# Kernel optimization log

Hardware: AMD Instinct MI355X
Metric: run time of the kernel (lower is better)

## Reference

```python
import jax, jax.numpy as jnp
import numpy as np

N_NODES = 100000
N_EDGES = 3200000
IN_DIM = 62
OUT_DIM = 16
EDGE_DIM = 2


def setup_inputs() -> dict:
    key = jax.random.key(0)
    ks = jax.random.split(key, 8)
    h = jax.random.normal(ks[0], (N_NODES, IN_DIM), dtype=jnp.float32)
    e = jax.random.normal(ks[1], (N_EDGES, EDGE_DIM), dtype=jnp.float32)
    src = jax.random.randint(ks[2], (N_EDGES,), 0, N_NODES, dtype=jnp.int32)
    dst = jax.random.randint(ks[3], (N_EDGES,), 0, N_NODES, dtype=jnp.int32)
    # xavier-normal-ish scaled weights
    W_fc = jax.random.normal(ks[4], (OUT_DIM, IN_DIM), dtype=jnp.float32) * 0.2
    W_attn = jax.random.normal(ks[5], (1, 2 * OUT_DIM + EDGE_DIM), dtype=jnp.float32) * 0.2
    W_edge = jax.random.normal(ks[6], (EDGE_DIM, EDGE_DIM), dtype=jnp.float32) * 0.5
    W_e2n = jax.random.normal(ks[7], (OUT_DIM, EDGE_DIM), dtype=jnp.float32) * 0.5
    return {"h": h, "e": e, "src": src, "dst": dst, "W_fc": W_fc,
            "W_attn": W_attn, "W_edge": W_edge, "W_e2n": W_e2n}


def _agat_forward(h, e, src, dst, W_fc, W_attn, W_edge, W_e2n):
    n = h.shape[0]
    d = W_fc.shape[0]
    z = h @ W_fc.T                      # [N, D]
    ex = e @ W_edge.T                   # [E, edge_dim]
    # attn_fc([z_src, z_dst, ex]) split into per-part projections
    Wa_src = W_attn[:, :d]              # [1, D]
    Wa_dst = W_attn[:, d:2 * d]         # [1, D]
    Wa_e = W_attn[:, 2 * d:]            # [1, edge_dim]
    a_src = (z @ Wa_src.T)[:, 0]        # [N] per-node, gathered per-edge
    a_dst = (z @ Wa_dst.T)[:, 0]        # [N]
    a = a_src[src] + a_dst[dst] + (ex @ Wa_e.T)[:, 0]   # [E]
    e_att = jax.nn.leaky_relu(a, negative_slope=0.01)    # [E]
    # segment softmax over incoming edges of each dst node
    m = jax.ops.segment_max(e_att, dst, num_segments=n)  # [N]
    w = jnp.exp(e_att - m[dst])                           # [E]
    denom = jax.ops.segment_sum(w, dst, num_segments=n)   # [N]
    attn = w / denom[dst]                                  # [E]
    # message = z_src + ez; aggregated as attn-weighted sum (matches
    # sum(attn*z) + sum(attn*ez) in reduce_func)
    ez = ex @ W_e2n.T                                      # [E, D]
    msg = attn[:, None] * (z[src] + ez)                    # [E, D]
    return jax.ops.segment_sum(msg, dst, num_segments=n)   # [N, D]


def reference(h, e, src, dst, W_fc, W_attn, W_edge, W_e2n):
    return _agat_forward(h, e, src, dst, W_fc, W_attn, W_edge, W_e2n)
```

## Files before the change

### kernel.cpp

```cpp
#include <hip/hip_runtime.h>
#include <hip/hip_fp16.h>

#define N_NODES 100000
#define N_EDGES 3200000
#define IN_DIM  62
#define OUT_DIM 16

#define EBC    6144
#define EPT    (EBC / 1024)
#define NEB    ((N_EDGES + EBC - 1) / EBC)
#define NPB    ((N_NODES + 1023) / 1024)
#define NBUCK  ((N_NODES + 63) / 64)
#define CSTR   16
#define ACCS   21
#define SZF    1048576.0f
#define SWF    16777216.0f
#define GTH    256

typedef int nat_i2 __attribute__((ext_vector_type(2)));

__device__ __forceinline__ unsigned fkey(float f) {
    unsigned b = __float_as_uint(f);
    return (b & 0x80000000u) ? ~b : (b | 0x80000000u);
}
__device__ __forceinline__ float finv(unsigned u) {
    unsigned b = (u & 0x80000000u) ? (u ^ 0x80000000u) : ~u;
    return __uint_as_float(b);
}

__global__ __launch_bounds__(1024) void proj_append_kernel(
    const float* __restrict__ h,
    const float* __restrict__ W_fc,
    const float* __restrict__ W_attn,
    const float* __restrict__ e,
    const int*   __restrict__ src,
    const int*   __restrict__ dst,
    __half* __restrict__ zh,
    float* __restrict__ a_src_arr,
    float* __restrict__ a_dst_arr,
    int*   __restrict__ cursor,
    nat_i2* __restrict__ records,
    int cap)
{
    __shared__ int  cnt[NBUCK];
    __shared__ int  pfx[NBUCK];
    __shared__ int  combo[NBUCK];
    __shared__ int2 pay[EBC];
    __shared__ unsigned short pbkt[EBC];
    __shared__ int  wsum[16];

    int tid = threadIdx.x;

    if (blockIdx.x < NPB) {
        int i = blockIdx.x * 1024 + tid;
        if (i >= N_NODES) return;

        float acc[OUT_DIM];
#pragma unroll
        for (int j = 0; j < OUT_DIM; ++j) acc[j] = 0.f;

        const float2* __restrict__ hr = (const float2*)(h + (size_t)i * IN_DIM);
#pragma unroll
        for (int kk = 0; kk < IN_DIM / 2; ++kk) {
            float2 hv = hr[kk];
#pragma unroll
            for (int j = 0; j < OUT_DIM; ++j) {
                acc[j] += hv.x * W_fc[j * IN_DIM + 2 * kk]
                        + hv.y * W_fc[j * IN_DIM + 2 * kk + 1];
            }
        }

        float asrc = 0.f, adst = 0.f;
#pragma unroll
        for (int j = 0; j < OUT_DIM; ++j) {
            asrc += acc[j] * W_attn[j];
            adst += acc[j] * W_attn[OUT_DIM + j];
        }

        union { __half hx[16]; uint4 q[2]; } u;
#pragma unroll
        for (int j = 0; j < OUT_DIM; ++j) u.hx[j] = __float2half(acc[j]);
        uint4* __restrict__ zrow = (uint4*)(zh + (size_t)i * OUT_DIM);
        zrow[0] = u.q[0];
        zrow[1] = u.q[1];

        a_src_arr[i] = asrc;
        a_dst_arr[i] = adst;
        return;
    }

    int be = blockIdx.x - NPB;
    long ebase = (long)be * EBC;
    int chunk_n = (int)min((long)EBC, (long)N_EDGES - ebase);

    int dv[EPT], sv[EPT];
    float2 ev[EPT];
#pragma unroll
    for (int j = 0; j < EPT; ++j) {
        int p = tid + j * 1024;
        dv[j] = -1;
        if (p < chunk_n) {
            long eid = ebase + p;
            dv[j] = dst[eid];
            sv[j] = src[eid];
            ev[j] = ((const float2*)e)[eid];
        }
    }

    for (int t = tid; t < NBUCK; t += 1024) cnt[t] = 0;
    __syncthreads();

#pragma unroll
    for (int j = 0; j < EPT; ++j)
        if (dv[j] >= 0) atomicAdd(&cnt[dv[j] >> 6], 1);
    __syncthreads();

    int b0 = 2 * tid, b1 = b0 + 1;
    int c0 = (b0 < NBUCK) ? cnt[b0] : 0;
    int c1 = (b1 < NBUCK) ? cnt[b1] : 0;
    if (b0 < NBUCK) cnt[b0] = 0;
    if (b1 < NBUCK) cnt[b1] = 0;
    int gb0 = 0, gb1 = 0;
    if (c0) gb0 = atomicAdd(&cursor[b0 * CSTR], c0);
    if (c1) gb1 = atomicAdd(&cursor[b1 * CSTR], c1);

    int ts = c0 + c1;
    {
        int lane = tid & 63, wid = tid >> 6;
        int x = ts;
#pragma unroll
        for (int off = 1; off < 64; off <<= 1) {
            int y = __shfl_up(x, off, 64);
            if (lane >= off) x += y;
        }
        if (lane == 63) wsum[wid] = x;
        __syncthreads();
        if (wid == 0) {
            int v = (lane < 16) ? wsum[lane] : 0;
#pragma unroll
            for (int off = 1; off < 16; off <<= 1) {
                int y = __shfl_up(v, off, 64);
                if (lane >= off) v += y;
            }
            if (lane < 16) wsum[lane] = v;
        }
        __syncthreads();
        int texcl = x - ts + (wid ? wsum[wid - 1] : 0);
        if (b0 < NBUCK) { pfx[b0] = texcl;      combo[b0] = b0 * cap + gb0 - texcl; }
        if (b1 < NBUCK) { pfx[b1] = texcl + c0; combo[b1] = b1 * cap + gb1 - (texcl + c0); }
    }
    __syncthreads();

#pragma unroll
    for (int j = 0; j < EPT; ++j) {
        if (dv[j] >= 0) {
            int b = dv[j] >> 6;
            union { __half2 h2; int i; } uu;
            uu.h2.x = __float2half(ev[j].x);
            uu.h2.y = __float2half(ev[j].y);
            int r = atomicAdd(&cnt[b], 1);
            int q = pfx[b] + r;
            pay[q]  = make_int2(uu.i, sv[j] | ((dv[j] & 63) << 17));
            pbkt[q] = (unsigned short)b;
        }
    }
    __syncthreads();

    for (int p = tid; p < chunk_n; p += 1024) {
        int2 v = pay[p];
        int bb = pbkt[p];
        int pos = combo[bb] + p;
        if (pos < (bb + 1) * cap) {
            nat_i2 vv; vv.x = v.x; vv.y = v.y;
            __builtin_nontemporal_store(vv, records + pos);
        }
    }
}

__global__ __launch_bounds__(GTH) void gather_fx_kernel(
    const int*    __restrict__ cursor,
    const nat_i2* __restrict__ records,
    const __half* __restrict__ zh,
    const float*  __restrict__ a_src_arr,
    const float*  __restrict__ a_dst_arr,
    const float*  __restrict__ W_attn,
    const float*  __restrict__ W_edge,
    const float*  __restrict__ W_e2n,
    float* __restrict__ out, int cap)
{
    __shared__ unsigned maxv[64];
    __shared__ int      acci[64 * ACCS];
    __shared__ float    adst_l[64];
    __shared__ float    we2n_s[2 * OUT_DIM];

    int b   = blockIdx.x;
    int tid = threadIdx.x;
    long lo = (long)b * cap;
    int n   = cursor[b * CSTR];
    int nl  = n < cap ? n : cap;

    if (tid < 64) {
        maxv[tid] = 0u;
        int node = (b << 6) + tid;
        adst_l[tid] = (node < N_NODES) ? a_dst_arr[node] : 0.f;
    }
    if (tid < 2 * OUT_DIM) we2n_s[tid] = W_e2n[tid];
    for (int t = tid; t < 64 * ACCS; t += GTH) acci[t] = 0;
    __syncthreads();

    float we00 = W_edge[0], we01 = W_edge[1], we10 = W_edge[2], we11 = W_edge[3];
    float wa0  = W_attn[2 * OUT_DIM], wa1 = W_attn[2 * OUT_DIM + 1];

    for (int k = tid; k < nl; k += GTH) {
        nat_i2 r = records[lo + k];
        int s  = r.y & 0x1FFFF;
        int ld = (r.y >> 17) & 63;
        union { int i; __half2 h2; } ue; ue.i = r.x;
        float e0 = __low2float(ue.h2), e1 = __high2float(ue.h2);
        float ex0 = e0 * we00 + e1 * we01;
        float ex1 = e0 * we10 + e1 * we11;
        float a  = a_src_arr[s] + adst_l[ld] + ex0 * wa0 + ex1 * wa1;
        float ea = (a > 0.f) ? a : 0.01f * a;
        atomicMax(&maxv[ld], fkey(ea));
    }
    __syncthreads();

    for (int k = tid; k < nl; k += GTH) {
        nat_i2 r = records[lo + k];
        int s  = r.y & 0x1FFFF;
        int ld = (r.y >> 17) & 63;
        union { int i; __half2 h2; } ue; ue.i = r.x;
        float e0 = __low2float(ue.h2), e1 = __high2float(ue.h2);
        float ex0 = e0 * we00 + e1 * we01;
        float ex1 = e0 * we10 + e1 * we11;
        float a  = a_src_arr[s] + adst_l[ld] + ex0 * wa0 + ex1 * wa1;
        float ea = (a > 0.f) ? a : 0.01f * a;
        float m  = finv(maxv[ld]);
        float w  = __expf(ea - m);

        const uint4* __restrict__ zr = (const uint4*)(zh + (size_t)s * OUT_DIM);
        uint4 z0 = zr[0], z1 = zr[1];

        int* ab = acci + ld * ACCS;
        union { unsigned u; __half2 h2; } t2;
        float ws = w * SZF;
        t2.u = z0.x; atomicAdd(ab + 0,  __float2int_rn(ws * __low2float(t2.h2)));
                     atomicAdd(ab + 1,  __float2int_rn(ws * __high2float(t2.h2)));
        t2.u = z0.y; atomicAdd(ab + 2,  __float2int_rn(ws * __low2float(t2.h2)));
                     atomicAdd(ab + 3,  __float2int_rn(ws * __high2float(t2.h2)));
        t2.u = z0.z; atomicAdd(ab + 4,  __float2int_rn(ws * __low2float(t2.h2)));
                     atomicAdd(ab + 5,  __float2int_rn(ws * __high2float(t2.h2)));
        t2.u = z0.w; atomicAdd(ab + 6,  __float2int_rn(ws * __low2float(t2.h2)));
                     atomicAdd(ab + 7,  __float2int_rn(ws * __high2float(t2.h2)));
        t2.u = z1.x; atomicAdd(ab + 8,  __float2int_rn(ws * __low2float(t2.h2)));
                     atomicAdd(ab + 9,  __float2int_rn(ws * __high2float(t2.h2)));
        t2.u = z1.y; atomicAdd(ab + 10, __float2int_rn(ws * __low2float(t2.h2)));
                     atomicAdd(ab + 11, __float2int_rn(ws * __high2float(t2.h2)));
        t2.u = z1.z; atomicAdd(ab + 12, __float2int_rn(ws * __low2float(t2.h2)));
                     atomicAdd(ab + 13, __float2int_rn(ws * __high2float(t2.h2)));
        t2.u = z1.w; atomicAdd(ab + 14, __float2int_rn(ws * __low2float(t2.h2)));
                     atomicAdd(ab + 15, __float2int_rn(ws * __high2float(t2.h2)));
        atomicAdd(ab + 16, __float2int_rn(w * SWF));
        atomicAdd(ab + 17, __float2int_rn(ws * ex0));
        atomicAdd(ab + 18, __float2int_rn(ws * ex1));
    }
    __syncthreads();

#pragma unroll
    for (int rp = 0; rp < 4; ++rp) {
        int idx  = rp * GTH + tid;
        int ln   = idx >> 4;
        int j    = idx & 15;
        int node = (b << 6) + ln;
        if (node < N_NODES) {
            const int* ab = acci + ln * ACCS;
            int swi = ab[16];
            float num  = (float)ab[j]  * (1.f / SZF);
            float ex0s = (float)ab[17] * (1.f / SZF);
            float ex1s = (float)ab[18] * (1.f / SZF);
            float ez   = ex0s * we2n_s[2 * j] + ex1s * we2n_s[2 * j + 1];
            float iv   = (swi != 0) ? (SWF / (float)swi) : 0.f;
            out[(size_t)node * OUT_DIM + j] = (num + ez) * iv;
        }
    }
}


__global__ __launch_bounds__(256) void node_proj_fb_kernel(
    const float* __restrict__ h,
    const float* __restrict__ W_fc,
    const float* __restrict__ W_attn,
    float* __restrict__ z,
    float* __restrict__ a_src_arr,
    float* __restrict__ a_dst_arr,
    float* __restrict__ denom,
    float* __restrict__ out)
{
    int i = blockIdx.x * blockDim.x + threadIdx.x;
    if (i >= N_NODES) return;

    float acc[OUT_DIM];
#pragma unroll
    for (int j = 0; j < OUT_DIM; ++j) acc[j] = 0.f;

    const float2* __restrict__ hr = (const float2*)(h + (size_t)i * IN_DIM);
#pragma unroll
    for (int kk = 0; kk < IN_DIM / 2; ++kk) {
        float2 hv = hr[kk];
#pragma unroll
        for (int j = 0; j < OUT_DIM; ++j) {
            acc[j] += hv.x * W_fc[j * IN_DIM + 2 * kk]
                    + hv.y * W_fc[j * IN_DIM + 2 * kk + 1];
        }
    }

    float asrc = 0.f, adst = 0.f;
#pragma unroll
    for (int j = 0; j < OUT_DIM; ++j) {
        asrc += acc[j] * W_attn[j];
        adst += acc[j] * W_attn[OUT_DIM + j];
    }

    float4* __restrict__ zrow = (float4*)(z + (size_t)i * OUT_DIM);
    zrow[0] = make_float4(acc[0],  acc[1],  acc[2],  acc[3]);
    zrow[1] = make_float4(acc[4],  acc[5],  acc[6],  acc[7]);
    zrow[2] = make_float4(acc[8],  acc[9],  acc[10], acc[11]);
    zrow[3] = make_float4(acc[12], acc[13], acc[14], acc[15]);

    a_src_arr[i] = asrc;
    a_dst_arr[i] = adst;
    denom[i] = 0.f;

    float4 z4 = make_float4(0.f, 0.f, 0.f, 0.f);
    float4* __restrict__ orow = (float4*)(out + (size_t)i * OUT_DIM);
    orow[0] = z4; orow[1] = z4; orow[2] = z4; orow[3] = z4;
}

__global__ __launch_bounds__(256) void edge_kernel(
    const float* __restrict__ e,
    const int*   __restrict__ src,
    const int*   __restrict__ dst,
    const float* __restrict__ W_attn,
    const float* __restrict__ W_edge,
    const float* __restrict__ W_e2n,
    const float* __restrict__ z,
    const float* __restrict__ a_src_arr,
    const float* __restrict__ a_dst_arr,
    float* __restrict__ denom,
    float* __restrict__ out)
{
    int eid = blockIdx.x * blockDim.x + threadIdx.x;
    if (eid >= N_EDGES) return;

    int s = src[eid];
    int d = dst[eid];

    float2 ev = ((const float2*)e)[eid];
    float ex0 = ev.x * W_edge[0] + ev.y * W_edge[1];
    float ex1 = ev.x * W_edge[2] + ev.y * W_edge[3];

    float a = a_src_arr[s] + a_dst_arr[d]
            + ex0 * W_attn[2 * OUT_DIM] + ex1 * W_attn[2 * OUT_DIM + 1];
    float ea = (a > 0.f) ? a : 0.01f * a;
    float w  = __expf(ea);

    unsafeAtomicAdd(denom + d, w);

    const float4* __restrict__ zrow = (const float4*)(z + (size_t)s * OUT_DIM);
    float4 z0 = zrow[0], z1 = zrow[1], z2 = zrow[2], z3 = zrow[3];

    float* __restrict__ orow = out + (size_t)d * OUT_DIM;
    float zs[OUT_DIM] = { z0.x, z0.y, z0.z, z0.w,
                          z1.x, z1.y, z1.z, z1.w,
                          z2.x, z2.y, z2.z, z2.w,
                          z3.x, z3.y, z3.z, z3.w };
#pragma unroll
    for (int j = 0; j < OUT_DIM; ++j) {
        float ez = ex0 * W_e2n[2 * j] + ex1 * W_e2n[2 * j + 1];
        unsafeAtomicAdd(orow + j, w * (zs[j] + ez));
    }
}

__global__ __launch_bounds__(256) void normalize_kernel(
    float* __restrict__ out, const float* __restrict__ denom)
{
    int tid = blockIdx.x * blockDim.x + threadIdx.x;
    const int total = N_NODES * OUT_DIM / 4;
    if (tid >= total) return;
    int n = tid >> 2;
    float dn = denom[n];
    float inv = (dn != 0.f) ? (1.f / dn) : 0.f;
    float4 v = ((float4*)out)[tid];
    v.x *= inv; v.y *= inv; v.z *= inv; v.w *= inv;
    ((float4*)out)[tid] = v;
}

extern "C" void kernel_launch(void* const* d_in, const int* in_sizes, int n_in,
                              void* d_out, int out_size, void* d_ws, size_t ws_size,
                              hipStream_t stream)
{
    const float* h      = (const float*)d_in[0];
    const float* e      = (const float*)d_in[1];
    const int*   src    = (const int*)  d_in[2];
    const int*   dst    = (const int*)  d_in[3];
    const float* W_fc   = (const float*)d_in[4];
    const float* W_attn = (const float*)d_in[5];
    const float* W_edge = (const float*)d_in[6];
    const float* W_e2n  = (const float*)d_in[7];
    float* out = (float*)d_out;

    char* ws = (char*)d_ws;

    size_t off = 0;
    __half* zh        = (__half*)(ws + off); off += (size_t)N_NODES * OUT_DIM * 2;
    float*  a_src_arr = (float*) (ws + off); off += (size_t)N_NODES * 4;
    float*  a_dst_arr = (float*) (ws + off); off += (size_t)N_NODES * 4;
    off = (off + 255) & ~(size_t)255;
    int*    cursor = (int*)(ws + off);
    size_t  cur_bytes = (size_t)NBUCK * CSTR * 4;
    off += (cur_bytes + 255) & ~(size_t)255;
    size_t rec_off = (off + 255) & ~(size_t)255;

    int cap = 0;
    if      (ws_size >= rec_off + (size_t)NBUCK * 4096 * 8) cap = 4096;
    else if (ws_size >= rec_off + (size_t)NBUCK * 3072 * 8) cap = 3072;
    else if (ws_size >= rec_off + (size_t)NBUCK * 2560 * 8) cap = 2560;
    else if (ws_size >= rec_off + (size_t)NBUCK * 2304 * 8) cap = 2304;

    if (cap) {
        nat_i2* records = (nat_i2*)(ws + rec_off);

        hipMemsetAsync(cursor, 0, cur_bytes, stream);

        proj_append_kernel<<<NPB + NEB, 1024, 0, stream>>>(
            h, W_fc, W_attn, e, src, dst,
            zh, a_src_arr, a_dst_arr, cursor, records, cap);

        gather_fx_kernel<<<NBUCK, GTH, 0, stream>>>(
            cursor, records, zh, a_src_arr, a_dst_arr,
            W_attn, W_edge, W_e2n, out, cap);
    } else {
        size_t foff = 0;
        float* z     = (float*)(ws + foff); foff += (size_t)N_NODES * OUT_DIM * 4;
        float* asrc  = (float*)(ws + foff); foff += (size_t)N_NODES * 4;
        float* adst  = (float*)(ws + foff); foff += (size_t)N_NODES * 4;
        float* denom = (float*)(ws + foff); foff += (size_t)N_NODES * 4;

        node_proj_fb_kernel<<<(N_NODES + 255) / 256, 256, 0, stream>>>(
            h, W_fc, W_attn, z, asrc, adst, denom, out);

        edge_kernel<<<(N_EDGES + 255) / 256, 256, 0, stream>>>(
            e, src, dst, W_attn, W_edge, W_e2n, z, asrc, adst, denom, out);

        normalize_kernel<<<(N_NODES * OUT_DIM / 4 + 255) / 256, 256, 0, stream>>>(
            out, denom);
    }
}
```

Measured before the change: 225.5 us.

## Fuse projection, bucketing and gather into one cooperative persistent kernel

Replaces the memset plus two-kernel pipeline with a single cooperative kernel. It zeroes the cursors, runs projection and edge bucketing in a grid-stride loop, syncs the grid, then runs the per-bucket gather. Buckets grow from 64 to 256 destination nodes with a larger per-bucket capacity, and blocks shrink to 256 threads with 2048-edge chunks. This removes launch gaps and the memset, but adds grid-sync cost and fewer, heavier gather blocks (391) with a large shared accumulator that may limit occupancy.

```diff
diff --git a/kernel.cpp b/kernel.cpp
--- a/kernel.cpp
+++ b/kernel.cpp
@@ -1,21 +1,26 @@
 #include <hip/hip_runtime.h>
 #include <hip/hip_fp16.h>
+#include <hip/hip_cooperative_groups.h>
+
+namespace cg = cooperative_groups;
 
 #define N_NODES 100000
 #define N_EDGES 3200000
 #define IN_DIM  62
 #define OUT_DIM 16
 
-#define EBC    6144
-#define EPT    (EBC / 1024)
+#define BTH    256
+#define EBC    2048
+#define EPT    8
 #define NEB    ((N_EDGES + EBC - 1) / EBC)
-#define NPB    ((N_NODES + 1023) / 1024)
-#define NBUCK  ((N_NODES + 63) / 64)
+#define BNODES 256
+#define NB2    ((N_NODES + BNODES - 1) / BNODES)
+#define NPU    NB2
 #define CSTR   16
 #define ACCS   21
 #define SZF    1048576.0f
 #define SWF    16777216.0f
-#define GTH    256
+#define NCU    256
 
 typedef int nat_i2 __attribute__((ext_vector_type(2)));
 
@@ -28,68 +33,73 @@
     return __uint_as_float(b);
 }
 
-__global__ __launch_bounds__(1024) void proj_append_kernel(
-    const float* __restrict__ h,
-    const float* __restrict__ W_fc,
+struct AppendSh {
+    int  cnt[NB2];
+    int  pfx[NB2];
+    int  combo[NB2];
+    int2 pay[EBC];
+    unsigned short pbkt[EBC];
+    int  wsum[BTH / 64];
+};
+struct GatherSh {
+    unsigned maxv[BNODES];
+    int      acci[BNODES * ACCS];
+    float    adst_l[BNODES];
+    float    we2n[2 * OUT_DIM];
+};
+union ShArena { AppendSh a; GatherSh g; };
+
+__device__ __forceinline__ void do_proj(
+    int u, int tid,
+    const float* __restrict__ h, const float* __restrict__ W_fc,
     const float* __restrict__ W_attn,
-    const float* __restrict__ e,
-    const int*   __restrict__ src,
-    const int*   __restrict__ dst,
-    __half* __restrict__ zh,
-    float* __restrict__ a_src_arr,
-    float* __restrict__ a_dst_arr,
-    int*   __restrict__ cursor,
-    nat_i2* __restrict__ records,
-    int cap)
-{
-    __shared__ int  cnt[NBUCK];
-    __shared__ int  pfx[NBUCK];
-    __shared__ int  combo[NBUCK];
-    __shared__ int2 pay[EBC];
-    __shared__ unsigned short pbkt[EBC];
-    __shared__ int  wsum[16];
-
-    int tid = threadIdx.x;
-
-    if (blockIdx.x < NPB) {
-        int i = blockIdx.x * 1024 + tid;
-        if (i >= N_NODES) return;
-
-        float acc[OUT_DIM];
-#pragma unroll
-        for (int j = 0; j < OUT_DIM; ++j) acc[j] = 0.f;
-
-        const float2* __restrict__ hr = (const float2*)(h + (size_t)i * IN_DIM);
-#pragma unroll
-        for (int kk = 0; kk < IN_DIM / 2; ++kk) {
-            float2 hv = hr[kk];
-#pragma unroll
-            for (int j = 0; j < OUT_DIM; ++j) {
-                acc[j] += hv.x * W_fc[j * IN_DIM + 2 * kk]
-                        + hv.y * W_fc[j * IN_DIM + 2 * kk + 1];
-            }
-        }
-
-        float asrc = 0.f, adst = 0.f;
+    __half* __restrict__ zh, float* __restrict__ a_src_arr,
+    float* __restrict__ a_dst_arr)
+{
+    int i = u * BTH + tid;
+    if (i >= N_NODES) return;
+
+    float acc[OUT_DIM];
+#pragma unroll
+    for (int j = 0; j < OUT_DIM; ++j) acc[j] = 0.f;
+
+    const float2* __restrict__ hr = (const float2*)(h + (size_t)i * IN_DIM);
+#pragma unroll
+    for (int kk = 0; kk < IN_DIM / 2; ++kk) {
+        float2 hv = hr[kk];
 #pragma unroll
         for (int j = 0; j < OUT_DIM; ++j) {
-            asrc += acc[j] * W_attn[j];
-            adst += acc[j] * W_attn[OUT_DIM + j];
-        }
-
-        union { __half hx[16]; uint4 q[2]; } u;
-#pragma unroll
-        for (int j = 0; j < OUT_DIM; ++j) u.hx[j] = __float2half(acc[j]);
-        uint4* __restrict__ zrow = (uint4*)(zh + (size_t)i * OUT_DIM);
-        zrow[0] = u.q[0];
-        zrow[1] = u.q[1];
-
-        a_src_arr[i] = asrc;
-        a_dst_arr[i] = adst;
-        return;
-    }
-
-    int be = blockIdx.x - NPB;
+            acc[j] += hv.x * W_fc[j * IN_DIM + 2 * kk]
+                    + hv.y * W_fc[j * IN_DIM + 2 * kk + 1];
+        }
+    }
+
+    float asrc = 0.f, adst = 0.f;
+#pragma unroll
+    for (int j = 0; j < OUT_DIM; ++j) {
+        asrc += acc[j] * W_attn[j];
+        adst += acc[j] * W_attn[OUT_DIM + j];
+    }
+
+    union { __half hx[16]; uint4 q[2]; } uq;
+#pragma unroll
+    for (int j = 0; j < OUT_DIM; ++j) uq.hx[j] = __float2half(acc[j]);
+    uint4* __restrict__ zrow = (uint4*)(zh + (size_t)i * OUT_DIM);
+    zrow[0] = uq.q[0];
+    zrow[1] = uq.q[1];
+
+    a_src_arr[i] = asrc;
+    a_dst_arr[i] = adst;
+}
+
+__device__ __forceinline__ void do_append(
+    int be, int tid, AppendSh& S,
+    const float* __restrict__ e, const int* __restrict__ src,
+    const int* __restrict__ dst, int* __restrict__ cursor,
+    nat_i2* __restrict__ records, int cap)
+{
+    __syncthreads();
+
     long ebase = (long)be * EBC;
     int chunk_n = (int)min((long)EBC, (long)N_EDGES - ebase);
 
@@ -97,7 +107,7 @@
     float2 ev[EPT];
 #pragma unroll
     for (int j = 0; j < EPT; ++j) {
-        int p = tid + j * 1024;
+        int p = tid + j * BTH;
         dv[j] = -1;
         if (p < chunk_n) {
             long eid = ebase + p;
@@ -107,19 +117,19 @@
         }
     }
 
-    for (int t = tid; t < NBUCK; t += 1024) cnt[t] = 0;
+    for (int t = tid; t < NB2; t += BTH) S.cnt[t] = 0;
     __syncthreads();
 
 #pragma unroll
     for (int j = 0; j < EPT; ++j)
-        if (dv[j] >= 0) atomicAdd(&cnt[dv[j] >> 6], 1);
+        if (dv[j] >= 0) atomicAdd(&S.cnt[dv[j] >> 8], 1);
     __syncthreads();
 
     int b0 = 2 * tid, b1 = b0 + 1;
-    int c0 = (b0 < NBUCK) ? cnt[b0] : 0;
-    int c1 = (b1 < NBUCK) ? cnt[b1] : 0;
-    if (b0 < NBUCK) cnt[b0] = 0;
-    if (b1 < NBUCK) cnt[b1] = 0;
+    int c0 = (b0 < NB2) ? S.cnt[b0] : 0;
+    int c1 = (b1 < NB2) ? S.cnt[b1] : 0;
+    if (b0 < NB2) S.cnt[b0] = 0;
+    if (b1 < NB2) S.cnt[b1] = 0;
     int gb0 = 0, gb1 = 0;
     if (c0) gb0 = atomicAdd(&cursor[b0 * CSTR], c0);
     if (c1) gb1 = atomicAdd(&cursor[b1 * CSTR], c1);
@@ -133,43 +143,41 @@
             int y = __shfl_up(x, off, 64);
             if (lane >= off) x += y;
         }
-        if (lane == 63) wsum[wid] = x;
+        if (lane == 63) S.wsum[wid] = x;
         __syncthreads();
-        if (wid == 0) {
-            int v = (lane < 16) ? wsum[lane] : 0;
-#pragma unroll
-            for (int off = 1; off < 16; off <<= 1) {
-                int y = __shfl_up(v, off, 64);
-                if (lane >= off) v += y;
+        if (tid == 0) {
+            int run = 0;
+#pragma unroll
+            for (int i2 = 0; i2 < BTH / 64; ++i2) {
+                int t = S.wsum[i2]; S.wsum[i2] = run; run += t;
             }
-            if (lane < 16) wsum[lane] = v;
         }
         __syncthreads();
-        int texcl = x - ts + (wid ? wsum[wid - 1] : 0);
-        if (b0 < NBUCK) { pfx[b0] = texcl;      combo[b0] = b0 * cap + gb0 - texcl; }
-        if (b1 < NBUCK) { pfx[b1] = texcl + c0; combo[b1] = b1 * cap + gb1 - (texcl + c0); }
+        int texcl = x - ts + S.wsum[wid];
+        if (b0 < NB2) { S.pfx[b0] = texcl;      S.combo[b0] = b0 * cap + gb0 - texcl; }
+        if (b1 < NB2) { S.pfx[b1] = texcl + c0; S.combo[b1] = b1 * cap + gb1 - (texcl + c0); }
     }
     __syncthreads();
 
 #pragma unroll
     for (int j = 0; j < EPT; ++j) {
         if (dv[j] >= 0) {
-            int b = dv[j] >> 6;
+            int b = dv[j] >> 8;
             union { __half2 h2; int i; } uu;
             uu.h2.x = __float2half(ev[j].x);
             uu.h2.y = __float2half(ev[j].y);
-            int r = atomicAdd(&cnt[b], 1);
-            int q = pfx[b] + r;
-            pay[q]  = make_int2(uu.i, sv[j] | ((dv[j] & 63) << 17));
-            pbkt[q] = (unsigned short)b;
-        }
-    }
-    __syncthreads();
-
-    for (int p = tid; p < chunk_n; p += 1024) {
-        int2 v = pay[p];
-        int bb = pbkt[p];
-        int pos = combo[bb] + p;
+            int r = atomicAdd(&S.cnt[b], 1);
+            int q = S.pfx[b] + r;
+            S.pay[q]  = make_int2(uu.i, sv[j] | ((dv[j] & (BNODES - 1)) << 17));
+            S.pbkt[q] = (unsigned short)b;
+        }
+    }
+    __syncthreads();
+
+    for (int p = tid; p < chunk_n; p += BTH) {
+        int2 v  = S.pay[p];
+        int  bb = S.pbkt[p];
+        int pos = S.combo[bb] + p;
         if (pos < (bb + 1) * cap) {
             nat_i2 vv; vv.x = v.x; vv.y = v.y;
             __builtin_nontemporal_store(vv, records + pos);
@@ -177,71 +185,63 @@
     }
 }
 
-__global__ __launch_bounds__(GTH) void gather_fx_kernel(
-    const int*    __restrict__ cursor,
-    const nat_i2* __restrict__ records,
-    const __half* __restrict__ zh,
-    const float*  __restrict__ a_src_arr,
-    const float*  __restrict__ a_dst_arr,
-    const float*  __restrict__ W_attn,
-    const float*  __restrict__ W_edge,
-    const float*  __restrict__ W_e2n,
+__device__ __forceinline__ void do_gather(
+    int b, int tid, GatherSh& G,
+    const int* __restrict__ cursor, const nat_i2* __restrict__ records,
+    const __half* __restrict__ zh, const float* __restrict__ a_src_arr,
+    const float* __restrict__ a_dst_arr, const float* __restrict__ W_attn,
+    const float* __restrict__ W_edge, const float* __restrict__ W_e2n,
     float* __restrict__ out, int cap)
 {
-    __shared__ unsigned maxv[64];
-    __shared__ int      acci[64 * ACCS];
-    __shared__ float    adst_l[64];
-    __shared__ float    we2n_s[2 * OUT_DIM];
-
-    int b   = blockIdx.x;
-    int tid = threadIdx.x;
+    __syncthreads();
+
     long lo = (long)b * cap;
     int n   = cursor[b * CSTR];
     int nl  = n < cap ? n : cap;
 
-    if (tid < 64) {
-        maxv[tid] = 0u;
-        int node = (b << 6) + tid;
-        adst_l[tid] = (node < N_NODES) ? a_dst_arr[node] : 0.f;
-    }
-    if (tid < 2 * OUT_DIM) we2n_s[tid] = W_e2n[tid];
-    for (int t = tid; t < 64 * ACCS; t += GTH) acci[t] = 0;
+    {
+        G.maxv[tid] = 0u;
+        int node = b * BNODES + tid;
+        G.adst_l[tid] = (node < N_NODES) ? a_dst_arr[node] : 0.f;
+        if (tid < 2 * OUT_DIM) G.we2n[tid] = W_e2n[tid];
+        for (int t = tid; t < BNODES * ACCS; t += BTH) G.acci[t] = 0;
+    }
     __syncthreads();
 
     float we00 = W_edge[0], we01 = W_edge[1], we10 = W_edge[2], we11 = W_edge[3];
     float wa0  = W_attn[2 * OUT_DIM], wa1 = W_attn[2 * OUT_DIM + 1];
 
-    for (int k = tid; k < nl; k += GTH) {
+    for (int k = tid; k < nl; k += BTH) {
         nat_i2 r = records[lo + k];
         int s  = r.y & 0x1FFFF;
-        int ld = (r.y >> 17) & 63;
+        int ld = (r.y >> 17) & 255;
         union { int i; __half2 h2; } ue; ue.i = r.x;
         float e0 = __low2float(ue.h2), e1 = __high2float(ue.h2);
         float ex0 = e0 * we00 + e1 * we01;
         float ex1 = e0 * we10 + e1 * we11;
-        float a  = a_src_arr[s] + adst_l[ld] + ex0 * wa0 + ex1 * wa1;
+        float a  = a_src_arr[s] + G.adst_l[ld] + ex0 * wa0 + ex1 * wa1;
         float ea = (a > 0.f) ? a : 0.01f * a;
-        atomicMax(&maxv[ld], fkey(ea));
-    }
-    __syncthreads();
-
-    for (int k = tid; k < nl; k += GTH) {
+        atomicMax(&G.maxv[ld], fkey(ea));
+    }
+    __syncthreads();
+
+    for (int k = tid; k < nl; k += BTH) {
         nat_i2 r = records[lo + k];
         int s  = r.y & 0x1FFFF;
-        int ld = (r.y >> 17) & 63;
+        int ld = (r.y >> 17) & 255;
         union { int i; __half2 h2; } ue; ue.i = r.x;
         float e0 = __low2float(ue.h2), e1 = __high2float(ue.h2);
         float ex0 = e0 * we00 + e1 * we01;
         float ex1 = e0 * we10 + e1 * we11;
-        float a  = a_src_arr[s] + adst_l[ld] + ex0 * wa0 + ex1 * wa1;
+        float a  = a_src_arr[s] + G.adst_l[ld] + ex0 * wa0 + ex1 * wa1;
         float ea = (a > 0.f) ? a : 0.01f * a;
-        float m  = finv(maxv[ld]);
+        float m  = finv(G.maxv[ld]);
         float w  = __expf(ea - m);
 
         const uint4* __restrict__ zr = (const uint4*)(zh + (size_t)s * OUT_DIM);
         uint4 z0 = zr[0], z1 = zr[1];
 
-        int* ab = acci + ld * ACCS;
+        int* ab = G.acci + ld * ACCS;
         union { unsigned u; __half2 h2; } t2;
         float ws = w * SZF;
         t2.u = z0.x; atomicAdd(ab + 0,  __float2int_rn(ws * __low2float(t2.h2)));
@@ -267,22 +267,77 @@
     __syncthreads();
 
 #pragma unroll
-    for (int rp = 0; rp < 4; ++rp) {
-        int idx  = rp * GTH + tid;
+    for (int rp = 0; rp < 16; ++rp) {
+        int idx  = rp * BTH + tid;
         int ln   = idx >> 4;
         int j    = idx & 15;
-        int node = (b << 6) + ln;
+        int node = b * BNODES + ln;
         if (node < N_NODES) {
-            const int* ab = acci + ln * ACCS;
+            const int* ab = G.acci + ln * ACCS;
             int swi = ab[16];
             float num  = (float)ab[j]  * (1.f / SZF);
             float ex0s = (float)ab[17] * (1.f / SZF);
             float ex1s = (float)ab[18] * (1.f / SZF);
-            float ez   = ex0s * we2n_s[2 * j] + ex1s * we2n_s[2 * j + 1];
+            float ez   = ex0s * G.we2n[2 * j] + ex1s * G.we2n[2 * j + 1];
             float iv   = (swi != 0) ? (SWF / (float)swi) : 0.f;
             out[(size_t)node * OUT_DIM + j] = (num + ez) * iv;
         }
     }
+}
+
+__global__ __launch_bounds__(BTH) void fused_kernel(
+    const float* __restrict__ h, const float* __restrict__ e,
+    const int* __restrict__ src, const int* __restrict__ dst,
+    const float* __restrict__ W_fc, const float* __restrict__ W_attn,
+    const float* __restrict__ W_edge, const float* __restrict__ W_e2n,
+    __half* __restrict__ zh, float* __restrict__ a_src_arr,
+    float* __restrict__ a_dst_arr, int* __restrict__ cursor,
+    nat_i2* __restrict__ records, float* __restrict__ out, int cap)
+{
+    __shared__ ShArena sh;
+    cg::grid_group grid = cg::this_grid();
+    int tid = threadIdx.x;
+
+    for (int t = blockIdx.x * BTH + tid; t < NB2 * CSTR; t += gridDim.x * BTH)
+        cursor[t] = 0;
+    grid.sync();
+
+    for (int u = blockIdx.x; u < NPU + NEB; u += gridDim.x) {
+        if (u < NPU) do_proj(u, tid, h, W_fc, W_attn, zh, a_src_arr, a_dst_arr);
+        else         do_append(u - NPU, tid, sh.a, e, src, dst, cursor, records, cap);
+    }
+    grid.sync();
+
+    for (int b = blockIdx.x; b < NB2; b += gridDim.x)
+        do_gather(b, tid, sh.g, cursor, records, zh, a_src_arr, a_dst_arr,
+                  W_attn, W_edge, W_e2n, out, cap);
+}
+
+__global__ __launch_bounds__(BTH) void proj_append_kernel(
+    const float* __restrict__ h, const float* __restrict__ W_fc,
+    const float* __restrict__ W_attn, const float* __restrict__ e,
+    const int* __restrict__ src, const int* __restrict__ dst,
+    __half* __restrict__ zh, float* __restrict__ a_src_arr,
+    float* __restrict__ a_dst_arr, int* __restrict__ cursor,
+    nat_i2* __restrict__ records, int cap)
+{
+    __shared__ AppendSh sh;
+    if (blockIdx.x < NPU)
+        do_proj(blockIdx.x, threadIdx.x, h, W_fc, W_attn, zh, a_src_arr, a_dst_arr);
+    else
+        do_append(blockIdx.x - NPU, threadIdx.x, sh, e, src, dst, cursor, records, cap);
+}
+
+__global__ __launch_bounds__(BTH) void gather_kernel(
+    const int* __restrict__ cursor, const nat_i2* __restrict__ records,
+    const __half* __restrict__ zh, const float* __restrict__ a_src_arr,
+    const float* __restrict__ a_dst_arr, const float* __restrict__ W_attn,
+    const float* __restrict__ W_edge, const float* __restrict__ W_e2n,
+    float* __restrict__ out, int cap)
+{
+    __shared__ GatherSh sh;
+    do_gather(blockIdx.x, threadIdx.x, sh, cursor, records, zh,
+              a_src_arr, a_dst_arr, W_attn, W_edge, W_e2n, out, cap);
 }
 
 
@@ -417,28 +472,47 @@
     float*  a_dst_arr = (float*) (ws + off); off += (size_t)N_NODES * 4;
     off = (off + 255) & ~(size_t)255;
     int*    cursor = (int*)(ws + off);
-    size_t  cur_bytes = (size_t)NBUCK * CSTR * 4;
+    size_t  cur_bytes = (size_t)NB2 * CSTR * 4;
     off += (cur_bytes + 255) & ~(size_t)255;
     size_t rec_off = (off + 255) & ~(size_t)255;
 
     int cap = 0;
-    if      (ws_size >= rec_off + (size_t)NBUCK * 4096 * 8) cap = 4096;
-    else if (ws_size >= rec_off + (size_t)NBUCK * 3072 * 8) cap = 3072;
-    else if (ws_size >= rec_off + (size_t)NBUCK * 2560 * 8) cap = 2560;
-    else if (ws_size >= rec_off + (size_t)NBUCK * 2304 * 8) cap = 2304;
+    if      (ws_size >= rec_off + (size_t)NB2 * 12288 * 8) cap = 12288;
+    else if (ws_size >= rec_off + (size_t)NB2 * 10240 * 8) cap = 10240;
+    else if (ws_size >= rec_off + (size_t)NB2 * 9216 * 8)  cap = 9216;
+    else if (ws_size >= rec_off + (size_t)NB2 * 8704 * 8)  cap = 8704;
 
     if (cap) {
         nat_i2* records = (nat_i2*)(ws + rec_off);
 
-        hipMemsetAsync(cursor, 0, cur_bytes, stream);
-
-        proj_append_kernel<<<NPB + NEB, 1024, 0, stream>>>(
-            h, W_fc, W_attn, e, src, dst,
-            zh, a_src_arr, a_dst_arr, cursor, records, cap);
-
-        gather_fx_kernel<<<NBUCK, GTH, 0, stream>>>(
-            cursor, records, zh, a_src_arr, a_dst_arr,
-            W_attn, W_edge, W_e2n, out, cap);
+        hipError_t lerr = hipErrorUnknown;
+        int maxB = 0;
+        hipError_t qerr = hipOccupancyMaxActiveBlocksPerMultiprocessor(
+            &maxB, reinterpret_cast<const void*>(fused_kernel), BTH, 0);
+        if (qerr == hipSuccess && maxB > 0) {
+            int gridB = maxB * NCU;
+            if (gridB > NPU + NEB) gridB = NPU + NEB;
+            void* kargs[] = {
+                (void*)&h, (void*)&e, (void*)&src, (void*)&dst,
+                (void*)&W_fc, (void*)&W_attn, (void*)&W_edge, (void*)&W_e2n,
+                (void*)&zh, (void*)&a_src_arr, (void*)&a_dst_arr,
+                (void*)&cursor, (void*)&records, (void*)&out, (void*)&cap };
+            lerr = hipLaunchCooperativeKernel(
+                reinterpret_cast<const void*>(fused_kernel),
+                dim3(gridB), dim3(BTH), kargs, 0, stream);
+        }
+
+        if (lerr != hipSuccess) {
+            hipMemsetAsync(cursor, 0, cur_bytes, stream);
+
+            proj_append_kernel<<<NPU + NEB, BTH, 0, stream>>>(
+                h, W_fc, W_attn, e, src, dst,
+                zh, a_src_arr, a_dst_arr, cursor, records, cap);
+
+            gather_kernel<<<NB2, BTH, 0, stream>>>(
+                cursor, records, zh, a_src_arr, a_dst_arr,
+                W_attn, W_edge, W_e2n, out, cap);
+        }
     } else {
         size_t foff = 0;
         float* z     = (float*)(ws + foff); foff += (size_t)N_NODES * OUT_DIM * 4;
```

After: 347.3 us. +54.0%, slower.

## Cache bucket edge records and attention scores in registers across softmax passes

Applied to the files above, without the earlier changes.

The per-bucket gather kernel now loads up to 16 edge records per thread into registers once, with a nontemporal load, and keeps the computed leaky-relu scores. The second pass reuses them instead of re-reading records and a_src from global memory and recomputing the score. It also batches the a_src gathers to expose memory-level parallelism. It assumes each bucket holds at most 16*256 records, and the added register arrays could lower occupancy.

```diff
diff --git a/kernel.cpp b/kernel.cpp
--- a/kernel.cpp
+++ b/kernel.cpp
@@ -16,6 +16,7 @@
 #define SZF    1048576.0f
 #define SWF    16777216.0f
 #define GTH    256
+#define EPTG   16
 
 typedef int nat_i2 __attribute__((ext_vector_type(2)));
 
@@ -211,58 +212,82 @@
     float we00 = W_edge[0], we01 = W_edge[1], we10 = W_edge[2], we11 = W_edge[3];
     float wa0  = W_attn[2 * OUT_DIM], wa1 = W_attn[2 * OUT_DIM + 1];
 
-    for (int k = tid; k < nl; k += GTH) {
-        nat_i2 r = records[lo + k];
-        int s  = r.y & 0x1FFFF;
-        int ld = (r.y >> 17) & 63;
-        union { int i; __half2 h2; } ue; ue.i = r.x;
-        float e0 = __low2float(ue.h2), e1 = __high2float(ue.h2);
-        float ex0 = e0 * we00 + e1 * we01;
-        float ex1 = e0 * we10 + e1 * we11;
-        float a  = a_src_arr[s] + adst_l[ld] + ex0 * wa0 + ex1 * wa1;
-        float ea = (a > 0.f) ? a : 0.01f * a;
-        atomicMax(&maxv[ld], fkey(ea));
-    }
-    __syncthreads();
-
-    for (int k = tid; k < nl; k += GTH) {
-        nat_i2 r = records[lo + k];
-        int s  = r.y & 0x1FFFF;
-        int ld = (r.y >> 17) & 63;
-        union { int i; __half2 h2; } ue; ue.i = r.x;
-        float e0 = __low2float(ue.h2), e1 = __high2float(ue.h2);
-        float ex0 = e0 * we00 + e1 * we01;
-        float ex1 = e0 * we10 + e1 * we11;
-        float a  = a_src_arr[s] + adst_l[ld] + ex0 * wa0 + ex1 * wa1;
-        float ea = (a > 0.f) ? a : 0.01f * a;
-        float m  = finv(maxv[ld]);
-        float w  = __expf(ea - m);
-
-        const uint4* __restrict__ zr = (const uint4*)(zh + (size_t)s * OUT_DIM);
-        uint4 z0 = zr[0], z1 = zr[1];
-
-        int* ab = acci + ld * ACCS;
-        union { unsigned u; __half2 h2; } t2;
-        float ws = w * SZF;
-        t2.u = z0.x; atomicAdd(ab + 0,  __float2int_rn(ws * __low2float(t2.h2)));
-                     atomicAdd(ab + 1,  __float2int_rn(ws * __high2float(t2.h2)));
-        t2.u = z0.y; atomicAdd(ab + 2,  __float2int_rn(ws * __low2float(t2.h2)));
-                     atomicAdd(ab + 3,  __float2int_rn(ws * __high2float(t2.h2)));
-        t2.u = z0.z; atomicAdd(ab + 4,  __float2int_rn(ws * __low2float(t2.h2)));
-                     atomicAdd(ab + 5,  __float2int_rn(ws * __high2float(t2.h2)));
-        t2.u = z0.w; atomicAdd(ab + 6,  __float2int_rn(ws * __low2float(t2.h2)));
-                     atomicAdd(ab + 7,  __float2int_rn(ws * __high2float(t2.h2)));
-        t2.u = z1.x; atomicAdd(ab + 8,  __float2int_rn(ws * __low2float(t2.h2)));
-                     atomicAdd(ab + 9,  __float2int_rn(ws * __high2float(t2.h2)));
-        t2.u = z1.y; atomicAdd(ab + 10, __float2int_rn(ws * __low2float(t2.h2)));
-                     atomicAdd(ab + 11, __float2int_rn(ws * __high2float(t2.h2)));
-        t2.u = z1.z; atomicAdd(ab + 12, __float2int_rn(ws * __low2float(t2.h2)));
-                     atomicAdd(ab + 13, __float2int_rn(ws * __high2float(t2.h2)));
-        t2.u = z1.w; atomicAdd(ab + 14, __float2int_rn(ws * __low2float(t2.h2)));
-                     atomicAdd(ab + 15, __float2int_rn(ws * __high2float(t2.h2)));
-        atomicAdd(ab + 16, __float2int_rn(w * SWF));
-        atomicAdd(ab + 17, __float2int_rn(ws * ex0));
-        atomicAdd(ab + 18, __float2int_rn(ws * ex1));
+    int   ry[EPTG];
+    int   eh[EPTG];
+    float ea[EPTG];
+
+#pragma unroll
+    for (int j = 0; j < EPTG; ++j) ry[j] = -1;
+
+#pragma unroll
+    for (int j = 0; j < EPTG; ++j) {
+        int k = tid + j * GTH;
+        if (k < nl) {
+            nat_i2 r = __builtin_nontemporal_load(records + lo + k);
+            ry[j] = r.y;
+            eh[j] = r.x;
+        }
+    }
+
+    float av[EPTG];
+#pragma unroll
+    for (int j = 0; j < EPTG; ++j)
+        if (ry[j] >= 0) av[j] = a_src_arr[ry[j] & 0x1FFFF];
+
+#pragma unroll
+    for (int j = 0; j < EPTG; ++j) {
+        if (ry[j] >= 0) {
+            int ld = (ry[j] >> 17) & 63;
+            union { int i; __half2 h2; } ue; ue.i = eh[j];
+            float e0 = __low2float(ue.h2), e1 = __high2float(ue.h2);
+            float ex0 = e0 * we00 + e1 * we01;
+            float ex1 = e0 * we10 + e1 * we11;
+            float a  = av[j] + adst_l[ld] + ex0 * wa0 + ex1 * wa1;
+            float eaj = (a > 0.f) ? a : 0.01f * a;
+            ea[j] = eaj;
+            atomicMax(&maxv[ld], fkey(eaj));
+        }
+    }
+    __syncthreads();
+
+#pragma unroll
+    for (int j = 0; j < EPTG; ++j) {
+        if (ry[j] >= 0) {
+            int s  = ry[j] & 0x1FFFF;
+            int ld = (ry[j] >> 17) & 63;
+            union { int i; __half2 h2; } ue; ue.i = eh[j];
+            float e0 = __low2float(ue.h2), e1 = __high2float(ue.h2);
+            float ex0 = e0 * we00 + e1 * we01;
+            float ex1 = e0 * we10 + e1 * we11;
+            float m = finv(maxv[ld]);
+            float w = __expf(ea[j] - m);
+
+            const uint4* __restrict__ zr = (const uint4*)(zh + (size_t)s * OUT_DIM);
+            uint4 z0 = zr[0], z1 = zr[1];
+
+            int* ab = acci + ld * ACCS;
+            union { unsigned u; __half2 h2; } t2;
+            float ws = w * SZF;
+            t2.u = z0.x; atomicAdd(ab + 0,  __float2int_rn(ws * __low2float(t2.h2)));
+                         atomicAdd(ab + 1,  __float2int_rn(ws * __high2float(t2.h2)));
+            t2.u = z0.y; atomicAdd(ab + 2,  __float2int_rn(ws * __low2float(t2.h2)));
+                         atomicAdd(ab + 3,  __float2int_rn(ws * __high2float(t2.h2)));
+            t2.u = z0.z; atomicAdd(ab + 4,  __float2int_rn(ws * __low2float(t2.h2)));
+                         atomicAdd(ab + 5,  __float2int_rn(ws * __high2float(t2.h2)));
+            t2.u = z0.w; atomicAdd(ab + 6,  __float2int_rn(ws * __low2float(t2.h2)));
+                         atomicAdd(ab + 7,  __float2int_rn(ws * __high2float(t2.h2)));
+            t2.u = z1.x; atomicAdd(ab + 8,  __float2int_rn(ws * __low2float(t2.h2)));
+                         atomicAdd(ab + 9,  __float2int_rn(ws * __high2float(t2.h2)));
+            t2.u = z1.y; atomicAdd(ab + 10, __float2int_rn(ws * __low2float(t2.h2)));
+                         atomicAdd(ab + 11, __float2int_rn(ws * __high2float(t2.h2)));
+            t2.u = z1.z; atomicAdd(ab + 12, __float2int_rn(ws * __low2float(t2.h2)));
+                         atomicAdd(ab + 13, __float2int_rn(ws * __high2float(t2.h2)));
+            t2.u = z1.w; atomicAdd(ab + 14, __float2int_rn(ws * __low2float(t2.h2)));
+                         atomicAdd(ab + 15, __float2int_rn(ws * __high2float(t2.h2)));
+            atomicAdd(ab + 16, __float2int_rn(w * SWF));
+            atomicAdd(ab + 17, __float2int_rn(ws * ex0));
+            atomicAdd(ab + 18, __float2int_rn(ws * ex1));
+        }
     }
     __syncthreads();
 
```

New measurement: 227.1 us. About the same (+0.7%).
